# Performance work log

Hardware: AMD Instinct MI355X
Metric: run time of the kernel (lower is better)

The kernel has to match this reference:

```python
import jax, jax.numpy as jnp
import numpy as np

B, H, W, CIN = 8, 32, 32, 64
COUT, NOUT, KH, KW = 64, 32, 3, 3


def setup_inputs() -> dict:
    key = jax.random.key(0)
    ks = jax.random.split(key, 7)
    n_flat = H * W * COUT  # conv output flattened (same padding, stride 1)
    return {
        "x": jax.random.normal(ks[0], (B, H, W, CIN), jnp.float32),
        "w_out_u": jax.random.normal(ks[1], (B, 1, n_flat, NOUT), jnp.float32) * 0.05,
        "b_out_u": jax.random.normal(ks[2], (B, 1, NOUT), jnp.float32),
        "w_out_l": jax.random.normal(ks[3], (B, 1, n_flat, NOUT), jnp.float32) * 0.05,
        "b_out_l": jax.random.normal(ks[4], (B, 1, NOUT), jnp.float32),
        "kernel": jax.random.normal(ks[5], (KH, KW, CIN, COUT), jnp.float32) * 0.1,
        "bias": jax.random.normal(ks[6], (COUT,), jnp.float32),
    }


def reference(x, w_out_u, b_out_u, w_out_l, b_out_l, kernel, bias):
    Bb, Hh, Ww, Cin = x.shape
    Cout = kernel.shape[-1]
    n_out = w_out_u.shape[-1]
    # 'same' padding, stride 1 -> conv output spatial dims equal input dims
    Ho, Wo = Hh, Ww

    # [B,1,n_flat,n_out] -> [B,n_out,Ho,Wo,Cout]
    wu = jnp.transpose(w_out_u, (0, 1, 3, 2)).reshape(Bb, n_out, Ho, Wo, Cout)
    wl = jnp.transpose(w_out_l, (0, 1, 3, 2)).reshape(Bb, n_out, Ho, Wo, Cout)

    # bias contribution: sum over spatial + channel -> [B, n_out] -> [B,1,n_out]
    b_u = jnp.sum(wu * bias, axis=(2, 3, 4))[:, None, :] + b_out_u
    b_l = jnp.sum(wl * bias, axis=(2, 3, 4))[:, None, :] + b_out_l

    # conv2d_transpose(z, kernel) == adjoint (vjp) of the forward conv.
    # Batch the per-n_out transposed convs (the K.rnn loop) into one call.
    def conv_fwd(z):  # z: [N,H,W,Cin] -> [N,Ho,Wo,Cout]
        return jax.lax.conv_general_dilated(
            z, kernel, window_strides=(1, 1), padding="SAME",
            dimension_numbers=("NHWC", "HWIO", "NHWC"))

    zeros_in = jnp.zeros((Bb * n_out, Hh, Ww, Cin), wu.dtype)
    _, vjp_fn = jax.vjp(conv_fwd, zeros_in)

    def conv_t(w):  # [B,n_out,Ho,Wo,Cout] -> [B,n_out,H,W,Cin]
        g = vjp_fn(w.reshape(Bb * n_out, Ho, Wo, Cout))[0]
        return g.reshape(Bb, n_out, Hh, Ww, Cin)

    wu_t = conv_t(wu)
    wl_t = conv_t(wl)

    n_in = Hh * Ww * Cin
    w_u_out = jnp.transpose(wu_t.reshape(Bb, 1, n_out, n_in), (0, 1, 3, 2))
    w_l_out = jnp.transpose(wl_t.reshape(Bb, 1, n_out, n_in), (0, 1, 3, 2))
    return (w_u_out, b_u, w_l_out, b_l)
```

## Files before the change

kernel.cpp:

```cpp
#include <hip/hip_runtime.h>
#include <cstdint>

typedef __attribute__((ext_vector_type(8))) short short8;
typedef __attribute__((ext_vector_type(16))) float f32x16;
typedef __attribute__((ext_vector_type(4))) unsigned int uint4v;

__device__ inline uint32_t f2bf(float f) {
    union { float f; uint32_t u; } x; x.f = f;
    return (x.u + 0x7FFF + ((x.u >> 16) & 1)) >> 16;
}
__device__ inline uint32_t fbits(float f) {
    union { float f; uint32_t u; } x; x.f = f;
    return x.u;
}
__device__ inline float bflo(uint32_t u) {
    union { uint32_t u; float f; } x; x.u = u << 16; return x.f;
}
__device__ inline float bfhi(uint32_t u) {
    union { uint32_t u; float f; } x; x.u = u & 0xFFFF0000u; return x.f;
}

__global__ __launch_bounds__(256) void k_xform(
    const float* __restrict__ wu, const float* __restrict__ wl,
    uint4v* __restrict__ X,
    const float* __restrict__ kk, uint4v* __restrict__ AF,
    const float* __restrict__ buI, const float* __restrict__ blI,
    float* __restrict__ buO, float* __restrict__ blO)
{
    int tid = blockIdx.x * 256 + threadIdx.x;

    if (tid < 512 + 4608) {
        if (tid < 256) buO[tid] = buI[tid];
        else if (tid < 512) blO[tid - 256] = blI[tid - 256];
        else {
            int a    = tid - 512;
            int al   = a & 63;
            int c    = (a >> 6) & 1;
            int kidx = (a >> 7) & 3;
            int tap  = a >> 9;
            const float* kp = kk + ((size_t)tap * 64 + c * 32 + (al & 31)) * 64
                                 + kidx * 16 + (al >> 5) * 8;
            uint4v w;
            #pragma unroll
            for (int pr = 0; pr < 4; pr++)
                w[pr] = f2bf(kp[2 * pr]) | (f2bf(kp[2 * pr + 1]) << 16);
            AF[((tap * 4 + kidx) * 2 + c) * 64 + al] = w;
        }
    }

    int l    = tid & 63;
    int kidx = (tid >> 6) & 3;
    int site = (tid >> 8) & 1023;
    int img  = tid >> 18;
    int b    = img >> 1;
    const float* src = (img & 1) ? wl : wu;
    int o = l & 31, ch = l >> 5;

    const float* p = src + ((size_t)b * 65536 + (size_t)site * 64
                            + kidx * 16 + ch * 8) * 32 + o;
    uint4v w;
    #pragma unroll
    for (int pr = 0; pr < 4; pr++) {
        float g0 = p[(2 * pr) * 32];
        float g1 = p[(2 * pr + 1) * 32];
        w[pr] = __builtin_amdgcn_perm(fbits(g1), fbits(g0), 0x07060302u);
    }
    X[tid] = w;
}

__global__ __launch_bounds__(256, 4) void k_conv(
    const uint16_t* __restrict__ X, const uint16_t* __restrict__ AF,
    const float* __restrict__ bias,
    float* __restrict__ outU, float* __restrict__ outL,
    float* __restrict__ buO, float* __restrict__ blO)
{
    int tdx  = threadIdx.x;
    int l    = tdx & 63;
    int wid  = tdx >> 6;
    int o    = l & 31;
    int ch   = l >> 5;
    int c    = wid >> 1;
    int wsel = wid & 1;

    int bid = blockIdx.x;
    int b   = bid & 7;
    int v   = bid >> 3;
    int h   = v & 31;
    int wq  = v >> 5;
    int w0  = wq * 4 + wsel * 2;

    bool sval[4] = { w0 != 0, true, true, w0 + 2 != 32 };
    const char* XB  = (const char*)X;
    const char* AFB = (const char*)AF;

    for (int UL = 0; UL < 2; UL++) {
        int img = b * 2 + UL;
        float* dst  = UL ? outL : outU;
        float* bdst = UL ? blO : buO;

        float bp = 0.f;
        f32x16 acc[2];
        acc[0] = (f32x16)0.f;
        acc[1] = (f32x16)0.f;

        for (int r = 0; r < 3; r++) {
            int hh = h + 1 - r;
            if ((unsigned)hh >= 32u) continue;

            const char* ps[4];
            #pragma unroll
            for (int si = 0; si < 4; si++) {
                int ww  = w0 - 1 + si;
                int wwc = ((unsigned)ww < 32u) ? ww : 0;
                ps[si] = XB + ((size_t)(img * 1024 + hh * 32 + wwc)) * 4096
                            + (size_t)l * 16;
            }

            #pragma unroll
            for (int kp2 = 0; kp2 < 2; kp2++) {
                uint4v bw[4][2];
                #pragma unroll
                for (int si = 0; si < 4; si++) {
                    if (sval[si]) {
                        #pragma unroll
                        for (int kj = 0; kj < 2; kj++)
                            bw[si][kj] = *(const uint4v*)(ps[si] + (2 * kp2 + kj) * 1024);
                    } else {
                        bw[si][0] = (uint4v)0u;
                        bw[si][1] = (uint4v)0u;
                    }
                }

                #pragma unroll
                for (int kj = 0; kj < 2; kj++) {
                    int kidx = 2 * kp2 + kj;
                    short8 A[3];
                    #pragma unroll
                    for (int kw = 0; kw < 3; kw++)
                        A[kw] = *(const short8*)(AFB
                                + (size_t)((((r * 3 + kw) * 4 + kidx) * 2 + c) * 64 + l) * 16);

                    if (r == 1 && c == 0) {
                        float4 b0 = *(const float4*)(bias + kidx * 16 + ch * 8);
                        float4 b1 = *(const float4*)(bias + kidx * 16 + ch * 8 + 4);
                        float bb[8] = {b0.x, b0.y, b0.z, b0.w, b1.x, b1.y, b1.z, b1.w};
                        #pragma unroll
                        for (int pr = 0; pr < 4; pr++) {
                            bp = fmaf(bflo(bw[1][kj][pr]), bb[2 * pr],
                                 fmaf(bfhi(bw[1][kj][pr]), bb[2 * pr + 1], bp));
                            bp = fmaf(bflo(bw[2][kj][pr]), bb[2 * pr],
                                 fmaf(bfhi(bw[2][kj][pr]), bb[2 * pr + 1], bp));
                        }
                    }

                    #pragma unroll
                    for (int si = 0; si < 4; si++) {
                        short8 Bf = __builtin_bit_cast(short8, bw[si][kj]);
                        #pragma unroll
                        for (int tw = 0; tw < 2; tw++) {
                            int kw = tw + 2 - si;
                            if (kw >= 0 && kw <= 2)
                                acc[tw] = __builtin_amdgcn_mfma_f32_32x32x16_bf16(
                                    A[kw], Bf, acc[tw], 0, 0, 0);
                        }
                    }
                }
            }
        }

        bp += __shfl_xor(bp, 32);
        if (l < 32 && c == 0) atomicAdd(&bdst[b * 32 + o], bp);

        #pragma unroll
        for (int tw = 0; tw < 2; tw++) {
            int w = w0 + tw;
            float* base = dst + ((size_t)b * 65536 + (size_t)(h * 32 + w) * 64 + c * 32) * 32;
            #pragma unroll
            for (int reg = 0; reg < 16; reg++) {
                int row = (reg & 3) + 8 * (reg >> 2) + 4 * (l >> 5);
                base[row * 32 + o] = acc[tw][reg];
            }
        }
    }
}

extern "C" void kernel_launch(void* const* d_in, const int* in_sizes, int n_in,
                              void* d_out, int out_size, void* d_ws, size_t ws_size,
                              hipStream_t stream) {
    const float* wu   = (const float*)d_in[1];
    const float* buI  = (const float*)d_in[2];
    const float* wl   = (const float*)d_in[3];
    const float* blI  = (const float*)d_in[4];
    const float* kk   = (const float*)d_in[5];
    const float* bias = (const float*)d_in[6];

    float* out  = (float*)d_out;
    float* outU = out;
    float* buO  = out + 16777216;
    float* outL = out + 16777216 + 256;
    float* blO  = out + 2 * 16777216 + 256;

    uint4v* AF = (uint4v*)d_ws;
    const size_t XOFF = 131072;
    uint4v* X = (uint4v*)((char*)d_ws + XOFF);

    k_xform<<<16384, 256, 0, stream>>>(wu, wl, X, kk, AF, buI, blI, buO, blO);
    k_conv<<<2048, 256, 0, stream>>>((const uint16_t*)X, (const uint16_t*)AF, bias,
                                     outU, outL, buO, blO);
}
```

Measured before the change: 106.8 us.

## Compute two output rows per block to reuse input row loads across kernel taps

Each block now computes two adjacent output rows instead of one and handles a single image (U or L) instead of looping over both. The four input rows feeding the pair are loaded once and reused across the overlapping kernel rows, which cuts input loads per output from three rows to two. Accumulator count doubles, so launch bounds drop from 4 to 3 waves per SIMD to leave room for registers, which lowers occupancy.

```diff
diff --git a/kernel.cpp b/kernel.cpp
--- a/kernel.cpp
+++ b/kernel.cpp
@@ -68,7 +68,7 @@
     X[tid] = w;
 }
 
-__global__ __launch_bounds__(256, 4) void k_conv(
+__global__ __launch_bounds__(256, 3) void k_conv(
     const uint16_t* __restrict__ X, const uint16_t* __restrict__ AF,
     const float* __restrict__ bias,
     float* __restrict__ outU, float* __restrict__ outL,
@@ -85,100 +85,112 @@
     int bid = blockIdx.x;
     int b   = bid & 7;
     int v   = bid >> 3;
-    int h   = v & 31;
-    int wq  = v >> 5;
+    int hp  = v & 15;
+    int wq  = (v >> 4) & 7;
+    int UL  = v >> 7;
+    int h0  = hp * 2;
     int w0  = wq * 4 + wsel * 2;
+    int img = b * 2 + UL;
+
+    float* dst  = UL ? outL : outU;
+    float* bdst = UL ? blO : buO;
 
     bool sval[4] = { w0 != 0, true, true, w0 + 2 != 32 };
     const char* XB  = (const char*)X;
     const char* AFB = (const char*)AF;
 
-    for (int UL = 0; UL < 2; UL++) {
-        int img = b * 2 + UL;
-        float* dst  = UL ? outL : outU;
-        float* bdst = UL ? blO : buO;
-
-        float bp = 0.f;
-        f32x16 acc[2];
-        acc[0] = (f32x16)0.f;
-        acc[1] = (f32x16)0.f;
-
-        for (int r = 0; r < 3; r++) {
-            int hh = h + 1 - r;
-            if ((unsigned)hh >= 32u) continue;
-
-            const char* ps[4];
+    float bp = 0.f;
+    f32x16 acc[2][2];
+    #pragma unroll
+    for (int ph = 0; ph < 2; ph++)
+        #pragma unroll
+        for (int tw = 0; tw < 2; tw++) acc[ph][tw] = (f32x16)0.f;
+
+    #pragma unroll
+    for (int j = 0; j < 4; j++) {
+        int hh = h0 + 2 - j;
+        if ((unsigned)hh >= 32u) continue;
+
+        const char* ps[4];
+        #pragma unroll
+        for (int si = 0; si < 4; si++) {
+            int ww  = w0 - 1 + si;
+            int wwc = ((unsigned)ww < 32u) ? ww : 0;
+            ps[si] = XB + ((size_t)(img * 1024 + hh * 32 + wwc)) * 4096
+                        + (size_t)l * 16;
+        }
+
+        #pragma unroll
+        for (int kp2 = 0; kp2 < 2; kp2++) {
+            uint4v bw[4][2];
             #pragma unroll
             for (int si = 0; si < 4; si++) {
-                int ww  = w0 - 1 + si;
-                int wwc = ((unsigned)ww < 32u) ? ww : 0;
-                ps[si] = XB + ((size_t)(img * 1024 + hh * 32 + wwc)) * 4096
-                            + (size_t)l * 16;
+                if (sval[si]) {
+                    #pragma unroll
+                    for (int kj = 0; kj < 2; kj++)
+                        bw[si][kj] = *(const uint4v*)(ps[si] + (2 * kp2 + kj) * 1024);
+                } else {
+                    bw[si][0] = (uint4v)0u;
+                    bw[si][1] = (uint4v)0u;
+                }
             }
 
             #pragma unroll
-            for (int kp2 = 0; kp2 < 2; kp2++) {
-                uint4v bw[4][2];
-                #pragma unroll
-                for (int si = 0; si < 4; si++) {
-                    if (sval[si]) {
-                        #pragma unroll
-                        for (int kj = 0; kj < 2; kj++)
-                            bw[si][kj] = *(const uint4v*)(ps[si] + (2 * kp2 + kj) * 1024);
-                    } else {
-                        bw[si][0] = (uint4v)0u;
-                        bw[si][1] = (uint4v)0u;
+            for (int kj = 0; kj < 2; kj++) {
+                int kidx = 2 * kp2 + kj;
+
+                if ((j == 1 || j == 2) && c == 0) {
+                    float4 b0 = *(const float4*)(bias + kidx * 16 + ch * 8);
+                    float4 b1 = *(const float4*)(bias + kidx * 16 + ch * 8 + 4);
+                    float bb[8] = {b0.x, b0.y, b0.z, b0.w, b1.x, b1.y, b1.z, b1.w};
+                    #pragma unroll
+                    for (int pr = 0; pr < 4; pr++) {
+                        bp = fmaf(bflo(bw[1][kj][pr]), bb[2 * pr],
+                             fmaf(bfhi(bw[1][kj][pr]), bb[2 * pr + 1], bp));
+                        bp = fmaf(bflo(bw[2][kj][pr]), bb[2 * pr],
+                             fmaf(bfhi(bw[2][kj][pr]), bb[2 * pr + 1], bp));
                     }
                 }
 
                 #pragma unroll
-                for (int kj = 0; kj < 2; kj++) {
-                    int kidx = 2 * kp2 + kj;
-                    short8 A[3];
-                    #pragma unroll
-                    for (int kw = 0; kw < 3; kw++)
-                        A[kw] = *(const short8*)(AFB
-                                + (size_t)((((r * 3 + kw) * 4 + kidx) * 2 + c) * 64 + l) * 16);
-
-                    if (r == 1 && c == 0) {
-                        float4 b0 = *(const float4*)(bias + kidx * 16 + ch * 8);
-                        float4 b1 = *(const float4*)(bias + kidx * 16 + ch * 8 + 4);
-                        float bb[8] = {b0.x, b0.y, b0.z, b0.w, b1.x, b1.y, b1.z, b1.w};
+                for (int ph = 0; ph < 2; ph++) {
+                    int r = ph + j - 1;
+                    if (r >= 0 && r <= 2) {
+                        short8 A[3];
                         #pragma unroll
-                        for (int pr = 0; pr < 4; pr++) {
-                            bp = fmaf(bflo(bw[1][kj][pr]), bb[2 * pr],
-                                 fmaf(bfhi(bw[1][kj][pr]), bb[2 * pr + 1], bp));
-                            bp = fmaf(bflo(bw[2][kj][pr]), bb[2 * pr],
-                                 fmaf(bfhi(bw[2][kj][pr]), bb[2 * pr + 1], bp));
-                        }
-                    }
-
-                    #pragma unroll
-                    for (int si = 0; si < 4; si++) {
-                        short8 Bf = __builtin_bit_cast(short8, bw[si][kj]);
+                        for (int kw = 0; kw < 3; kw++)
+                            A[kw] = *(const short8*)(AFB
+                                    + (size_t)((((r * 3 + kw) * 4 + kidx) * 2 + c) * 64 + l) * 16);
                         #pragma unroll
-                        for (int tw = 0; tw < 2; tw++) {
-                            int kw = tw + 2 - si;
-                            if (kw >= 0 && kw <= 2)
-                                acc[tw] = __builtin_amdgcn_mfma_f32_32x32x16_bf16(
-                                    A[kw], Bf, acc[tw], 0, 0, 0);
+                        for (int si = 0; si < 4; si++) {
+                            short8 Bf = __builtin_bit_cast(short8, bw[si][kj]);
+                            #pragma unroll
+                            for (int tw = 0; tw < 2; tw++) {
+                                int kw = tw + 2 - si;
+                                if (kw >= 0 && kw <= 2)
+                                    acc[ph][tw] = __builtin_amdgcn_mfma_f32_32x32x16_bf16(
+                                        A[kw], Bf, acc[ph][tw], 0, 0, 0);
+                            }
                         }
                     }
                 }
             }
         }
-
-        bp += __shfl_xor(bp, 32);
-        if (l < 32 && c == 0) atomicAdd(&bdst[b * 32 + o], bp);
-
+    }
+
+    bp += __shfl_xor(bp, 32);
+    if (l < 32 && c == 0) atomicAdd(&bdst[b * 32 + o], bp);
+
+    #pragma unroll
+    for (int ph = 0; ph < 2; ph++) {
         #pragma unroll
         for (int tw = 0; tw < 2; tw++) {
-            int w = w0 + tw;
+            int h = h0 + ph, w = w0 + tw;
             float* base = dst + ((size_t)b * 65536 + (size_t)(h * 32 + w) * 64 + c * 32) * 32;
             #pragma unroll
             for (int reg = 0; reg < 16; reg++) {
                 int row = (reg & 3) + 8 * (reg >> 2) + 4 * (l >> 5);
-                base[row * 32 + o] = acc[tw][reg];
+                base[row * 32 + o] = acc[ph][tw][reg];
             }
         }
     }
```

Result: no change. 105.1 us (-1.5%).
